# Performance work log

Hardware: AMD Instinct MI355X
Metric: run time of the kernel (lower is better)

The kernel has to match this reference:

```python
import jax, jax.numpy as jnp
import numpy as np

LAM = 0.5   # dec_init_lambda
NEG = -1e8  # attention mask fill


def gru_cell(x, h, W_ih, W_hh, b_ih, b_hh):
    # torch.nn.GRUCell math
    gi = x @ W_ih.T + b_ih
    gh = h @ W_hh.T + b_hh
    ir, iz, inn = jnp.split(gi, 3, axis=-1)
    hr, hz, hn = jnp.split(gh, 3, axis=-1)
    r = jax.nn.sigmoid(ir + hr)
    z = jax.nn.sigmoid(iz + hz)
    n = jnp.tanh(inn + r * hn)
    return (1.0 - z) * n + z * h


def setup_inputs() -> dict:
    key = jax.random.key(0)
    S, B, C, H, E, V, TY = 64, 64, 512, 512, 512, 32000, 49
    ks = jax.random.split(key, 16)
    sc = lambda d: 1.0 / float(np.sqrt(d))
    inp = {}
    inp['ctx'] = jax.random.normal(ks[0], (S, B, C), jnp.float32)
    inp['ctx_mask'] = jnp.ones((S, B), jnp.float32)
    inp['txt_ctx'] = jax.random.normal(ks[1], (B, C), jnp.float32)
    inp['y'] = jax.random.randint(ks[2], (TY, B), 0, V)
    emb = jax.random.normal(ks[3], (V, E), jnp.float32) * 0.01
    inp['emb_table'] = emb.at[0].set(0.0)  # padding_idx=0
    inp['W_ctx2ctx'] = jax.random.normal(ks[4], (C, C), jnp.float32) * sc(C)
    inp['W_hid2ctx'] = jax.random.normal(ks[5], (C, H), jnp.float32) * sc(H)
    inp['w_mlp'] = jax.random.normal(ks[6], (C,), jnp.float32) * sc(C)
    inp['W_ctx2hid'] = jax.random.normal(ks[7], (H, C), jnp.float32) * sc(C)
    inp['W_dec_init'] = jax.random.normal(ks[8], (H, C), jnp.float32) * sc(C)
    inp['W_ih0'] = jax.random.normal(ks[9], (3 * H, E), jnp.float32) * sc(E)
    inp['W_hh0'] = jax.random.normal(ks[10], (3 * H, H), jnp.float32) * sc(H)
    inp['b_ih0'] = jnp.zeros((3 * H,), jnp.float32)
    inp['b_hh0'] = jnp.zeros((3 * H,), jnp.float32)
    inp['W_ih1'] = jax.random.normal(ks[11], (3 * H, H), jnp.float32) * sc(H)
    inp['W_hh1'] = jax.random.normal(ks[12], (3 * H, H), jnp.float32) * sc(H)
    inp['b_ih1'] = jnp.zeros((3 * H,), jnp.float32)
    inp['b_hh1'] = jnp.zeros((3 * H,), jnp.float32)
    inp['W_hid2out'] = jax.random.normal(ks[13], (E, H), jnp.float32) * sc(H)
    inp['b_hid2out'] = jnp.zeros((E,), jnp.float32)  # bias_zero=True
    inp['W_out2prob'] = jax.random.normal(ks[14], (V, E), jnp.float32) * sc(E)
    inp['b_out2prob'] = jnp.zeros((V,), jnp.float32)
    return inp


def reference(ctx, ctx_mask, txt_ctx, y, emb_table,
              W_ctx2ctx, W_hid2ctx, w_mlp, W_ctx2hid, W_dec_init,
              W_ih0, W_hh0, b_ih0, b_hh0,
              W_ih1, W_hh1, b_ih1, b_hh1,
              W_hid2out, b_hid2out, W_out2prob, b_out2prob):
    # f_init: mix mean visual ctx with sentence ctx, project to h0
    mean_ctx = ctx.sum(0) / ctx_mask.sum(0)[:, None]          # (B, C)
    mixed = LAM * mean_ctx + (1.0 - LAM) * txt_ctx            # (B, C)
    h0 = jnp.tanh(mixed @ W_dec_init.T)                       # (B, H)

    # precompute ctx projection of MLP attention (ctx2ctx), shared across steps
    ctx_proj = jnp.einsum('sbc,mc->sbm', ctx, W_ctx2ctx)      # (S, B, C)

    x_seq = emb_table[y[:-1]]                                 # (T, B, E) teacher-forced inputs
    tgt = y[1:]                                               # (T, B) targets

    def step(h, xs):
        x, t = xs
        h1 = gru_cell(x, h, W_ih0, W_hh0, b_ih0, b_hh0)       # (B, H)
        q = h1 @ W_hid2ctx.T                                  # (B, C)
        scores = jnp.einsum('sbm,m->sb', jnp.tanh(ctx_proj + q[None]), w_mlp)
        scores = jnp.where(ctx_mask > 0, scores, NEG)
        alpha = jax.nn.softmax(scores, axis=0)                # (S, B) over source
        z_t = jnp.einsum('sb,sbc->bc', alpha, ctx) @ W_ctx2hid.T  # (B, H)
        h2 = gru_cell(z_t, h1, W_ih1, W_hh1, b_ih1, b_hh1)    # (B, H)
        logit = jnp.tanh(h2 @ W_hid2out.T + b_hid2out)        # (B, E)
        log_p = jax.nn.log_softmax(logit @ W_out2prob.T + b_out2prob, axis=-1)
        lp = jnp.take_along_axis(log_p, t[:, None], axis=1)[:, 0]
        loss_t = -jnp.where(t != 0, lp, 0.0).sum()            # NLLLoss(sum, ignore_index=0)
        return h2, loss_t

    _, losses = jax.lax.scan(step, h0, (x_seq, tgt))
    return losses.sum()
```

## Files before the change

### kernel.cpp

```cpp
#include <hip/hip_runtime.h>
#include <stdint.h>


using bf16x8 = __attribute__((ext_vector_type(8))) short;
using f32x4  = __attribute__((ext_vector_type(4))) float;
using s16x4  = __attribute__((ext_vector_type(4))) short;
typedef unsigned long long u64;
typedef unsigned int u32;

#define DI __device__ __forceinline__

DI short f2bf(float x){
  union { float f; uint32_t u; } v; v.f = x;
  uint32_t r = (v.u + 0x7FFFu + ((v.u >> 16) & 1u)) >> 16;
  return (short)r;
}
DI float bf2f(short s){
  union { uint32_t u; float f; } v; v.u = ((uint32_t)(unsigned short)s) << 16; return v.f;
}
DI float sigm(float x){ return __fdividef(1.f, 1.f + __expf(-x)); }
DI float ftanh(float x){ return 1.f - __fdividef(2.f, __expf(2.f*x) + 1.f); }
DI float wsum(float v){
  #pragma unroll
  for (int m = 32; m > 0; m >>= 1) v += __shfl_xor(v, m, 64);
  return v;
}
DI f32x4 mfma16(bf16x8 a, bf16x8 b, f32x4 c){
  return __builtin_amdgcn_mfma_f32_16x16x32_bf16(a, b, c, 0, 0, 0);
}

DI u32  ald32(const u32* p){ return __hip_atomic_load(p, __ATOMIC_RELAXED, __HIP_MEMORY_SCOPE_AGENT); }
DI void ast32(u32* p, u32 v){ __hip_atomic_store(p, v, __ATOMIC_RELAXED, __HIP_MEMORY_SCOPE_AGENT); }
DI u64  ald64(const u64* p){ return __hip_atomic_load(p, __ATOMIC_RELAXED, __HIP_MEMORY_SCOPE_AGENT); }
DI void ast64(u64* p, u64 v){ __hip_atomic_store(p, v, __ATOMIC_RELAXED, __HIP_MEMORY_SCOPE_AGENT); }
DI float aldf(const float* p){ return __hip_atomic_load(p, __ATOMIC_RELAXED, __HIP_MEMORY_SCOPE_AGENT); }
DI void astf(float* p, float v){ __hip_atomic_store(p, v, __ATOMIC_RELAXED, __HIP_MEMORY_SCOPE_AGENT); }

DI bf16x8 ldb(const short* __restrict__ W, int n0, int k0, int lane){
  return *(const bf16x8*)(W + (size_t)(n0 + (lane & 15)) * 512 + k0 + ((lane >> 4) << 3));
}

#define SLOT 64

DI void sig(u32* arr, int slot, u32 tok){
  if (threadIdx.x == 0){
    __builtin_amdgcn_s_waitcnt(0);
    ast32(arr + slot * SLOT, tok);
  }
}
DI void waitslots(const u32* arr, int base, int cnt, u32 tok){
  if (threadIdx.x < 64){
    for (;;){
      u32 v = (threadIdx.x < cnt) ? ald32(arr + (base + threadIdx.x) * SLOT) : tok;
      if (__all((int)(v - tok) >= 0)) break;
      __builtin_amdgcn_s_sleep(2);
    }
  }
  __syncthreads();
}


struct CvtJobs { const float* src[8]; short* dst[8]; int cum4[9]; };

__global__ __launch_bounds__(256) void k_cvt_multi(CvtJobs jb, int total4){
  int i = blockIdx.x * 256 + threadIdx.x;
  if (i >= total4) return;
  int j = 0;
  #pragma unroll
  for (int k = 0; k < 8; ++k) if (i >= jb.cum4[k + 1]) j = k + 1;
  int off = i - jb.cum4[j];
  float4 v = ((const float4*)jb.src[j])[off];
  s16x4 o; o[0] = f2bf(v.x); o[1] = f2bf(v.y); o[2] = f2bf(v.z); o[3] = f2bf(v.w);
  ((s16x4*)jb.dst[j])[off] = o;
}

__global__ __launch_bounds__(256) void k_tc(const float* __restrict__ W, short* __restrict__ WT){
  int i = blockIdx.x * 256 + threadIdx.x;
  int c = i >> 9, h = i & 511;
  WT[i] = f2bf(W[h * 512 + c]);
}

__global__ __launch_bounds__(256) void k_zero(float* __restrict__ p, int n){
  int i = blockIdx.x * 256 + threadIdx.x;
  if (i < n) p[i] = 0.f;
}

__global__ __launch_bounds__(256) void k_meanmix(const float* __restrict__ ctx, const float* __restrict__ mask,
                                                 const float* __restrict__ txt, float* __restrict__ mixed){
  int i = blockIdx.x * 256 + threadIdx.x;
  int b = i >> 9, c = i & 511;
  float s = 0.f;
  for (int t = 0; t < 64; ++t) s += ctx[(size_t)(t * 64 + b) * 512 + c];
  float dn = 0.f;
  for (int t = 0; t < 64; ++t) dn += mask[t * 64 + b];
  mixed[i] = 0.5f * (s / dn) + 0.5f * txt[i];
}

__global__ __launch_bounds__(256) void k_pack_h0(const float* __restrict__ h0, u32* __restrict__ hbf){
  int i = blockIdx.x * 256 + threadIdx.x;
  u32 lo = (u32)(unsigned short)f2bf(h0[2 * i]);
  u32 hi = (u32)(unsigned short)f2bf(h0[2 * i + 1]);
  hbf[i] = lo | (hi << 16);
}


DI bf16x8 load_a32(const float* __restrict__ A, int ld, int m0, int k0, int lane){
  const float* p = A + (size_t)(m0 + (lane & 15)) * ld + k0 + ((lane >> 4) << 3);
  bf16x8 f;
  #pragma unroll
  for (int j = 0; j < 8; ++j) f[j] = f2bf(p[j]);
  return f;
}

__global__ __launch_bounds__(256) void k_gemm_bt(const float* __restrict__ A, const short* __restrict__ W,
                                                 float* __restrict__ C, int N, int act){
  int wg = blockIdx.x * 4 + (threadIdx.x >> 6);
  int lane = threadIdx.x & 63;
  int ntiles = N >> 4;
  int mt = wg / ntiles, nt = wg - mt * ntiles;
  int m0 = mt << 4, n0 = nt << 4;
  f32x4 acc = {0.f, 0.f, 0.f, 0.f};
  for (int k = 0; k < 512; k += 32)
    acc = mfma16(load_a32(A, 512, m0, k, lane), ldb(W, n0, k, lane), acc);
  int col = n0 + (lane & 15);
  int r0 = m0 + ((lane >> 4) << 2);
  #pragma unroll
  for (int r = 0; r < 4; ++r){
    float v = acc[r];
    if (act) v = ftanh(v);
    C[(size_t)(r0 + r) * N + col] = v;
  }
}

__global__ __launch_bounds__(256) void k_gemm_bt_obf(const float* __restrict__ A, const short* __restrict__ W,
                                                     short* __restrict__ C, int N){
  int wg = blockIdx.x * 4 + (threadIdx.x >> 6);
  int lane = threadIdx.x & 63;
  int ntiles = N >> 4;
  int mt = wg / ntiles, nt = wg - mt * ntiles;
  int m0 = mt << 4, n0 = nt << 4;
  f32x4 acc = {0.f, 0.f, 0.f, 0.f};
  for (int k = 0; k < 512; k += 32)
    acc = mfma16(load_a32(A, 512, m0, k, lane), ldb(W, n0, k, lane), acc);
  int col = n0 + (lane & 15);
  int r0 = m0 + ((lane >> 4) << 2);
  #pragma unroll
  for (int r = 0; r < 4; ++r)
    C[(size_t)(r0 + r) * N + col] = f2bf(acc[r]);
}

__global__ __launch_bounds__(256) void k_gi0(const int* __restrict__ y, const float* __restrict__ emb,
                                             const short* __restrict__ W, const float* __restrict__ bias,
                                             float* __restrict__ C){
  int wg = blockIdx.x * 4 + (threadIdx.x >> 6);
  int lane = threadIdx.x & 63;
  int mt = wg / 96, nt = wg - mt * 96;
  int m0 = mt << 4, n0 = nt << 4;
  int yr = y[m0 + (lane & 15)];
  const float* arow = emb + (size_t)yr * 512;
  f32x4 acc = {0.f, 0.f, 0.f, 0.f};
  for (int k = 0; k < 512; k += 32){
    const float* p = arow + k + ((lane >> 4) << 3);
    bf16x8 a;
    #pragma unroll
    for (int j = 0; j < 8; ++j) a[j] = f2bf(p[j]);
    acc = mfma16(a, ldb(W, n0, k, lane), acc);
  }
  int col = n0 + (lane & 15);
  int r0 = m0 + ((lane >> 4) << 2);
  #pragma unroll
  for (int r = 0; r < 4; ++r)
    C[(size_t)(r0 + r) * 1536 + col] = acc[r] + bias[col];
}


struct RB {
  const float* gi0;
  const short* Whh0; const float* bhh0;
  const short* Whid2ctx;
  const short* Whh1; const float* bhh1;
  const short* Wcomb; const float* bih1;
  const short* ctx_proj;
  const float* ctx;
  const float* mask;
  const float* wmlp;
  unsigned short* h_bf;
  unsigned short* h1_bf;
  unsigned short* catt_bf;
  float* qpart;
  float* h2;
  u32* barA; u32* barC; u32* barD;
};

__global__ __launch_bounds__(256, 1) void k_recur(RB a){
  __shared__ unsigned short sH[16 * 520];
  __shared__ float sOut[16 * 64];
  __shared__ float qs[512];
  __shared__ float wm[512];
  __shared__ float sc[64], al[64];
  const int wg = blockIdx.x, tid = threadIdx.x;
  const int wv = tid >> 6, lane = tid & 63;

  wm[tid] = a.wmlp[tid]; wm[tid + 256] = a.wmlp[tid + 256];
  __syncthreads();

  auto burst16 = [&](const unsigned short* src, int row0){
    #pragma unroll
    for (int i = 0; i < 8; ++i){
      int idx = tid + i * 256;
      int r = idx >> 7, c4 = idx & 127;
      u64 v = ald64((const u64*)(src + (size_t)(row0 + r) * 512) + c4);
      *(u64*)(sH + r * 520 + c4 * 4) = v;
    }
    __syncthreads();
  };
  auto afrag = [&](int k0) -> bf16x8 {
    return *(const bf16x8*)(sH + (lane & 15) * 520 + k0 + ((lane >> 4) << 3));
  };
  auto packstore = [&](unsigned short* dst, int mrow0, int jbase){
    int r = tid >> 4, ch = tid & 15;
    float4 v = *(const float4*)&sOut[r * 64 + ch * 4];
    u64 pk = (u64)(unsigned short)f2bf(v.x)
           | ((u64)(unsigned short)f2bf(v.y) << 16)
           | ((u64)(unsigned short)f2bf(v.z) << 32)
           | ((u64)(unsigned short)f2bf(v.w) << 48);
    ast64((u64*)(dst + (size_t)(mrow0 + r) * 512 + jbase + ch * 4), pk);
  };
  auto attention = [&](int b){
    float q0 = 0.f, q1 = 0.f;
    #pragma unroll
    for (int cgi = 0; cgi < 8; ++cgi){
      u64 v = ald64((const u64*)(a.qpart + (size_t)(cgi * 64 + b) * 512) + tid);
      union { u64 u; float f[2]; } cv; cv.u = v;
      q0 += cv.f[0]; q1 += cv.f[1];
    }
    qs[2 * tid] = q0; qs[2 * tid + 1] = q1;
    __syncthreads();
    for (int i = 0; i < 16; ++i){
      int s = (wv << 4) + i;
      const short* cp = a.ctx_proj + (size_t)((s << 6) + b) * 512 + lane * 8;
      bf16x8 c8 = *(const bf16x8*)cp;
      float p = 0.f;
      #pragma unroll
      for (int j = 0; j < 8; ++j){
        int m = lane * 8 + j;
        p += ftanh(bf2f(c8[j]) + qs[m]) * wm[m];
      }
      p = wsum(p);
      if (lane == 0) sc[s] = p;
    }
    __syncthreads();
    if (tid < 64){
      float mk = a.mask[(tid << 6) + b];
      float v = (mk > 0.f) ? sc[tid] : -100000000.0f;
      float mx = v;
      #pragma unroll
      for (int m = 32; m > 0; m >>= 1) mx = fmaxf(mx, __shfl_xor(mx, m, 64));
      float e = __expf(v - mx);
      float se = e;
      #pragma unroll
      for (int m = 32; m > 0; m >>= 1) se += __shfl_xor(se, m, 64);
      al[tid] = e / se;
    }
    __syncthreads();
    float s0 = 0.f, s1 = 0.f;
    int c0 = tid * 2;
    for (int s = 0; s < 64; ++s){
      float2 cv = *(const float2*)(a.ctx + (size_t)((s << 6) + b) * 512 + c0);
      s0 += al[s] * cv.x; s1 += al[s] * cv.y;
    }
    u32 pk = (u32)(unsigned short)f2bf(s0) | ((u32)(unsigned short)f2bf(s1) << 16);
    ast32((u32*)a.catt_bf + (size_t)b * 256 + tid, pk);
  };

  if (wg < 32){
    const int rg = wg >> 3, cg = wg & 7;
    const int mrow0 = rg << 4, jbase = cg << 6;
    const int j0 = jbase + (wv << 4);
    const int col = j0 + (lane & 15), lcol = col - jbase;
    const int lr0 = (lane >> 4) << 2;
    const int batt = wg;
    const int abase = (batt >> 4) << 3;
    #pragma unroll 1
    for (int t = 0; t < 48; ++t){
      const u32 tok = t + 1;
      waitslots(a.barD, rg << 3, 8, (u32)t);
      burst16(a.h_bf, mrow0);
      const float* gi = a.gi0 + (size_t)t * 98304;
      float giv0[4], giv1[4], giv2[4];
      #pragma unroll
      for (int r = 0; r < 4; ++r){
        const float* gib = gi + (size_t)(mrow0 + lr0 + r) * 1536;
        giv0[r] = gib[col]; giv1[r] = gib[512 + col]; giv2[r] = gib[1024 + col];
      }
      f32x4 aR = {0,0,0,0}, aZ = {0,0,0,0}, aN = {0,0,0,0};
      for (int k0 = 0; k0 < 512; k0 += 32){
        bf16x8 af = afrag(k0);
        aR = mfma16(af, ldb(a.Whh0, j0,        k0, lane), aR);
        aZ = mfma16(af, ldb(a.Whh0, 512 + j0,  k0, lane), aZ);
        aN = mfma16(af, ldb(a.Whh0, 1024 + j0, k0, lane), aN);
      }
      #pragma unroll
      for (int r = 0; r < 4; ++r){
        int lr = lr0 + r;
        float rr = sigm(giv0[r] + aR[r] + a.bhh0[col]);
        float zz = sigm(giv1[r] + aZ[r] + a.bhh0[512 + col]);
        float nn = ftanh(giv2[r] + rr * (aN[r] + a.bhh0[1024 + col]));
        float hp = bf2f((short)sH[lr * 520 + col]);
        sOut[lr * 64 + lcol] = (1.f - zz) * nn + zz * hp;
      }
      __syncthreads();
      packstore(a.h1_bf, mrow0, jbase);
      bf16x8 qa0, qa1;
      #pragma unroll
      for (int j = 0; j < 8; ++j){
        qa0[j] = f2bf(sOut[(lane & 15) * 64 +      ((lane >> 4) << 3) + j]);
        qa1[j] = f2bf(sOut[(lane & 15) * 64 + 32 + ((lane >> 4) << 3) + j]);
      }
      #pragma unroll
      for (int nt = 0; nt < 8; ++nt){
        int n0 = (wv << 7) + (nt << 4);
        f32x4 qacc = {0,0,0,0};
        qacc = mfma16(qa0, ldb(a.Whid2ctx, n0, jbase,      lane), qacc);
        qacc = mfma16(qa1, ldb(a.Whid2ctx, n0, jbase + 32, lane), qacc);
        int qcol = n0 + (lane & 15);
        #pragma unroll
        for (int r = 0; r < 4; ++r)
          astf(a.qpart + (size_t)(cg * 64 + mrow0 + lr0 + r) * 512 + qcol, qacc[r]);
      }
      __syncthreads();
      sig(a.barA, wg, tok);
      waitslots(a.barA, abase, 8, tok);
      attention(batt);
      __syncthreads();
      sig(a.barC, batt, tok);
    }
  } else if (wg < 64){
    const int g = wg - 32;
    const int rg = g >> 3, cg = g & 7;
    const int mrow0 = rg << 4, jbase = cg << 6;
    const int j0 = jbase + (wv << 4);
    const int col = j0 + (lane & 15), lcol = col - jbase;
    const int lr0 = (lane >> 4) << 2;
    #pragma unroll 1
    for (int t = 0; t < 48; ++t){
      const u32 tok = t + 1;
      waitslots(a.barA, rg << 3, 8, tok);
      burst16(a.h1_bf, mrow0);
      f32x4 hR = {0,0,0,0}, hZ = {0,0,0,0}, hN = {0,0,0,0};
      for (int k0 = 0; k0 < 512; k0 += 32){
        bf16x8 af = afrag(k0);
        hR = mfma16(af, ldb(a.Whh1, j0,        k0, lane), hR);
        hZ = mfma16(af, ldb(a.Whh1, 512 + j0,  k0, lane), hZ);
        hN = mfma16(af, ldb(a.Whh1, 1024 + j0, k0, lane), hN);
      }
      float hp4[4];
      #pragma unroll
      for (int r = 0; r < 4; ++r) hp4[r] = bf2f((short)sH[(lr0 + r) * 520 + col]);
      waitslots(a.barC, mrow0, 16, tok);
      burst16(a.catt_bf, mrow0);
      f32x4 iR = {0,0,0,0}, iZ = {0,0,0,0}, iN = {0,0,0,0};
      for (int k0 = 0; k0 < 512; k0 += 32){
        bf16x8 af = afrag(k0);
        iR = mfma16(af, ldb(a.Wcomb, j0,        k0, lane), iR);
        iZ = mfma16(af, ldb(a.Wcomb, 512 + j0,  k0, lane), iZ);
        iN = mfma16(af, ldb(a.Wcomb, 1024 + j0, k0, lane), iN);
      }
      float* h2t = a.h2 + (size_t)t * 32768;
      #pragma unroll
      for (int r = 0; r < 4; ++r){
        int lr = lr0 + r, b = mrow0 + lr;
        float rr = sigm(iR[r] + a.bih1[col]        + hR[r] + a.bhh1[col]);
        float zz = sigm(iZ[r] + a.bih1[512 + col]  + hZ[r] + a.bhh1[512 + col]);
        float nn = ftanh(iN[r] + a.bih1[1024 + col] + rr * (hN[r] + a.bhh1[1024 + col]));
        float hv = (1.f - zz) * nn + zz * hp4[r];
        h2t[(size_t)b * 512 + col] = hv;
        sOut[lr * 64 + lcol] = hv;
      }
      __syncthreads();
      packstore(a.h_bf, mrow0, jbase);
      __syncthreads();
      sig(a.barD, g, tok);
    }
  } else {
    const int b = wg - 32;
    const int abase = (b >> 4) << 3;
    #pragma unroll 1
    for (int t = 0; t < 48; ++t){
      const u32 tok = t + 1;
      waitslots(a.barA, abase, 8, tok);
      attention(b);
      __syncthreads();
      sig(a.barC, b, tok);
    }
  }
}


__global__ __launch_bounds__(256) void k_logit(const float* __restrict__ A, const short* __restrict__ W,
                                               const float* __restrict__ bias, short* __restrict__ tlb,
                                               float* __restrict__ tlf){
  int wg = blockIdx.x * 4 + (threadIdx.x >> 6);
  int lane = threadIdx.x & 63;
  int mt = wg >> 5, nt = wg & 31;
  int m0 = mt << 4, n0 = nt << 4;
  f32x4 acc = {0.f, 0.f, 0.f, 0.f};
  for (int k = 0; k < 512; k += 32)
    acc = mfma16(load_a32(A, 512, m0, k, lane), ldb(W, n0, k, lane), acc);
  int col = n0 + (lane & 15);
  int r0 = m0 + ((lane >> 4) << 2);
  #pragma unroll
  for (int r = 0; r < 4; ++r){
    float v = ftanh(acc[r] + bias[col]);
    size_t o = (size_t)(r0 + r) * 512 + col;
    tlf[o] = v; tlb[o] = f2bf(v);
  }
}

__global__ __launch_bounds__(256) void k_sumexp(const short* __restrict__ A, const short* __restrict__ B,
                                                const float* __restrict__ bias, float* __restrict__ sumexp){
  __shared__ short lA[128 * 40];
  __shared__ short lB[128 * 40];
  int bm = blockIdx.x % 24, bn = blockIdx.x / 24;
  int m0 = bm * 128, n0 = bn * 128;
  int tid = threadIdx.x, w = tid >> 6, lane = tid & 63;
  int mq = (w >> 1) * 64, nq = (w & 1) * 64;
  f32x4 acc[4][4];
  #pragma unroll
  for (int i = 0; i < 4; ++i)
    #pragma unroll
    for (int j = 0; j < 4; ++j) acc[i][j] = (f32x4){0.f, 0.f, 0.f, 0.f};

  for (int k0 = 0; k0 < 512; k0 += 32){
    __syncthreads();
    #pragma unroll
    for (int i = 0; i < 2; ++i){
      int idx = tid * 8 + i * 2048;
      int row = idx >> 5, colh = idx & 31;
      *(bf16x8*)&lA[row * 40 + colh] = *(const bf16x8*)(A + (size_t)(m0 + row) * 512 + k0 + colh);
      *(bf16x8*)&lB[row * 40 + colh] = *(const bf16x8*)(B + (size_t)(n0 + row) * 512 + k0 + colh);
    }
    __syncthreads();
    bf16x8 af[4], bfr[4];
    #pragma unroll
    for (int x = 0; x < 4; ++x){
      af[x]  = *(const bf16x8*)&lA[(mq + x * 16 + (lane & 15)) * 40 + ((lane >> 4) << 3)];
      bfr[x] = *(const bf16x8*)&lB[(nq + x * 16 + (lane & 15)) * 40 + ((lane >> 4) << 3)];
    }
    #pragma unroll
    for (int mi = 0; mi < 4; ++mi)
      #pragma unroll
      for (int ni = 0; ni < 4; ++ni)
        acc[mi][ni] = mfma16(af[mi], bfr[ni], acc[mi][ni]);
  }

  #pragma unroll
  for (int mi = 0; mi < 4; ++mi){
    #pragma unroll
    for (int r = 0; r < 4; ++r){
      float e = 0.f;
      #pragma unroll
      for (int ni = 0; ni < 4; ++ni){
        int col = n0 + nq + ni * 16 + (lane & 15);
        e += __expf(acc[mi][ni][r] + bias[col]);
      }
      e += __shfl_xor(e, 1, 64); e += __shfl_xor(e, 2, 64);
      e += __shfl_xor(e, 4, 64); e += __shfl_xor(e, 8, 64);
      if ((lane & 15) == 0){
        int row = m0 + mq + mi * 16 + ((lane >> 4) << 2) + r;
        atomicAdd(&sumexp[row], e);
      }
    }
  }
}

__global__ __launch_bounds__(256) void k_loss(const float* __restrict__ tlf, const float* __restrict__ Wop,
                                              const float* __restrict__ bop, const int* __restrict__ y,
                                              const float* __restrict__ sumexp, float* __restrict__ loss){
  int step = blockIdx.x;
  int w = threadIdx.x >> 6, lane = threadIdx.x & 63;
  __shared__ float accw[4];
  float part = 0.f;
  for (int b = w; b < 64; b += 4){
    int row = step * 64 + b;
    int t = y[(step + 1) * 64 + b];
    if (t != 0){
      const float* a = tlf + (size_t)row * 512 + lane * 8;
      const float* wr = Wop + (size_t)t * 512 + lane * 8;
      float d = 0.f;
      #pragma unroll
      for (int j = 0; j < 8; ++j) d += a[j] * wr[j];
      d = wsum(d);
      if (lane == 0) part += d + bop[t] - __logf(sumexp[row]);
    }
  }
  if (lane == 0) accw[w] = part;
  __syncthreads();
  if (threadIdx.x == 0) atomicAdd(loss, -(accw[0] + accw[1] + accw[2] + accw[3]));
}

__global__ void k_final(const float* __restrict__ loss, float* __restrict__ out){
  if (threadIdx.x == 0 && blockIdx.x == 0) out[0] = loss[0];
}


extern "C" void kernel_launch(void* const* d_in, const int* in_sizes, int n_in,
                              void* d_out, int out_size, void* d_ws, size_t ws_size,
                              hipStream_t stream) {
  const float* ctx       = (const float*)d_in[0];
  const float* ctx_mask  = (const float*)d_in[1];
  const float* txt_ctx   = (const float*)d_in[2];
  const int*   y         = (const int*)d_in[3];
  const float* emb       = (const float*)d_in[4];
  const float* W_ctx2ctx = (const float*)d_in[5];
  const float* W_hid2ctx = (const float*)d_in[6];
  const float* w_mlp     = (const float*)d_in[7];
  const float* W_ctx2hid = (const float*)d_in[8];
  const float* W_dec_init= (const float*)d_in[9];
  const float* W_ih0     = (const float*)d_in[10];
  const float* W_hh0     = (const float*)d_in[11];
  const float* b_ih0     = (const float*)d_in[12];
  const float* b_hh0     = (const float*)d_in[13];
  const float* W_ih1     = (const float*)d_in[14];
  const float* W_hh1     = (const float*)d_in[15];
  const float* b_ih1     = (const float*)d_in[16];
  const float* b_hh1     = (const float*)d_in[17];
  const float* W_hid2out = (const float*)d_in[18];
  const float* b_hid2out = (const float*)d_in[19];
  const float* W_out2prob= (const float*)d_in[20];
  const float* b_out2prob= (const float*)d_in[21];
  float* out = (float*)d_out;

  char* p = (char*)d_ws;
  auto alloc = [&](size_t n){ char* r = p; p += (n + 255) & ~(size_t)255; return r; };
  short* Wb_hh0     = (short*)alloc((size_t)1536 * 512 * 2);
  short* Wb_hid2ctx = (short*)alloc((size_t)512 * 512 * 2);
  short* Wb_hh1     = (short*)alloc((size_t)1536 * 512 * 2);
  short* Wb_hid2out = (short*)alloc((size_t)512 * 512 * 2);
  short* Wb_dec     = (short*)alloc((size_t)512 * 512 * 2);
  short* Wb_c2c     = (short*)alloc((size_t)512 * 512 * 2);
  short* Wb_ih0     = (short*)alloc((size_t)1536 * 512 * 2);
  short* Wb_o2p     = (short*)alloc((size_t)32000 * 512 * 2);
  short* WctT       = (short*)alloc((size_t)512 * 512 * 2);
  short* Wb_comb    = (short*)alloc((size_t)1536 * 512 * 2);
  short* ctx_projbf = (short*)alloc((size_t)4096 * 512 * 2);
  float* gi0_all    = (float*)alloc((size_t)3072 * 1536 * 4);
  float* mixed      = (float*)alloc((size_t)64 * 512 * 4);
  float* h0buf      = (float*)alloc((size_t)64 * 512 * 4);
  unsigned short* h_bf    = (unsigned short*)alloc((size_t)64 * 512 * 2);
  unsigned short* h1_bf   = (unsigned short*)alloc((size_t)64 * 512 * 2);
  unsigned short* catt_bf = (unsigned short*)alloc((size_t)64 * 512 * 2);
  float* qpart      = (float*)alloc((size_t)8 * 64 * 512 * 4);
  float* h2_all     = (float*)alloc((size_t)3072 * 512 * 4);
  short* tl_bf      = (short*)alloc((size_t)3072 * 512 * 2);
  float* tl_f       = (float*)alloc((size_t)3072 * 512 * 4);
  int nbar = 3 * 64 * SLOT;
  float* zreg       = (float*)alloc((size_t)(3073 + nbar) * 4);
  float* sumexp     = zreg;
  float* lossbuf    = zreg + 3072;
  u32* barA         = (u32*)(zreg + 3073);
  u32* barC         = barA + 64 * SLOT;
  u32* barD         = barC + 64 * SLOT;

  dim3 blk(256);
  CvtJobs jb;
  const float* srcs[8] = {W_hh0, W_hid2ctx, W_hh1, W_hid2out, W_dec_init, W_ctx2ctx, W_ih0, W_out2prob};
  short* dsts[8] = {Wb_hh0, Wb_hid2ctx, Wb_hh1, Wb_hid2out, Wb_dec, Wb_c2c, Wb_ih0, Wb_o2p};
  int sizes4[8] = {1536*512/4, 512*512/4, 1536*512/4, 512*512/4, 512*512/4, 512*512/4, 1536*512/4, 32000*512/4};
  int cum = 0;
  for (int i = 0; i < 8; ++i){ jb.src[i] = srcs[i]; jb.dst[i] = dsts[i]; jb.cum4[i] = cum; cum += sizes4[i]; }
  jb.cum4[8] = cum;
  k_cvt_multi<<<dim3((cum + 255) / 256), blk, 0, stream>>>(jb, cum);
  k_tc<<<dim3(1024), blk, 0, stream>>>(W_ctx2hid, WctT);
  k_gemm_bt_obf<<<dim3(768), blk, 0, stream>>>(W_ih1, WctT, Wb_comb, 512);
  k_meanmix<<<dim3(128), blk, 0, stream>>>(ctx, ctx_mask, txt_ctx, mixed);
  k_gemm_bt<<<dim3(32), blk, 0, stream>>>(mixed, Wb_dec, h0buf, 512, 1);
  k_pack_h0<<<dim3(64), blk, 0, stream>>>(h0buf, (u32*)h_bf);
  k_gemm_bt_obf<<<dim3(2048), blk, 0, stream>>>(ctx, Wb_c2c, ctx_projbf, 512);
  k_gi0<<<dim3(4608), blk, 0, stream>>>(y, emb, Wb_ih0, b_ih0, gi0_all);
  k_zero<<<dim3((3073 + nbar + 255) / 256), blk, 0, stream>>>(zreg, 3073 + nbar);

  RB rb;
  rb.gi0 = gi0_all;
  rb.Whh0 = Wb_hh0; rb.bhh0 = b_hh0;
  rb.Whid2ctx = Wb_hid2ctx;
  rb.Whh1 = Wb_hh1; rb.bhh1 = b_hh1;
  rb.Wcomb = Wb_comb; rb.bih1 = b_ih1;
  rb.ctx_proj = ctx_projbf; rb.ctx = ctx; rb.mask = ctx_mask; rb.wmlp = w_mlp;
  rb.h_bf = h_bf; rb.h1_bf = h1_bf; rb.catt_bf = catt_bf;
  rb.qpart = qpart; rb.h2 = h2_all;
  rb.barA = barA; rb.barC = barC; rb.barD = barD;
  void* kargs[] = { &rb };
  hipLaunchCooperativeKernel((const void*)k_recur, dim3(96), blk, kargs, 0, stream);

  k_logit<<<dim3(1536), blk, 0, stream>>>(h2_all, Wb_hid2out, b_hid2out, tl_bf, tl_f);
  k_sumexp<<<dim3(6000), blk, 0, stream>>>(tl_bf, Wb_o2p, b_out2prob, sumexp);
  k_loss<<<dim3(48), blk, 0, stream>>>(tl_f, W_out2prob, b_out2prob, y, sumexp, lossbuf);
  k_final<<<dim3(1), blk, 0, stream>>>(lossbuf, out);
}
```

Measured before the change: 2.761 ms.

## Tune recurrent kernel: register-cached params, gi prefetch, LDS attention reduce, block swizzle

Several independent tweaks to the persistent recurrent kernel. Bias, w_mlp and mask values are loaded once into registers, and the next step's input-gate values are prefetched after the attention signal so the load is off the critical path. The per-source wave reductions are replaced by writing partial dot products to reused shared memory and summing rows per thread, and the spin-wait sleep is shortened. The sum-exp GEMM also gets a block-index swizzle meant to improve cache locality.

Result: faster. 2.552 ms (-7.6%).

```diff
diff --git a/kernel.cpp b/kernel.cpp
--- a/kernel.cpp
+++ b/kernel.cpp
@@ -53,7 +53,7 @@
     for (;;){
       u32 v = (threadIdx.x < cnt) ? ald32(arr + (base + threadIdx.x) * SLOT) : tok;
       if (__all((int)(v - tok) >= 0)) break;
-      __builtin_amdgcn_s_sleep(2);
+      __builtin_amdgcn_s_sleep(1);
     }
   }
   __syncthreads();
@@ -193,16 +193,14 @@
 };
 
 __global__ __launch_bounds__(256, 1) void k_recur(RB a){
-  __shared__ unsigned short sH[16 * 520];
-  __shared__ float sOut[16 * 64];
+  __shared__ char smem[16 * 520 * 2 + 16 * 64 * 4];
+  unsigned short* sH = (unsigned short*)smem;
+  float* sOut = (float*)(smem + 16 * 520 * 2);
+  float* pl   = (float*)smem;
   __shared__ float qs[512];
-  __shared__ float wm[512];
-  __shared__ float sc[64], al[64];
+  __shared__ float al[64];
   const int wg = blockIdx.x, tid = threadIdx.x;
   const int wv = tid >> 6, lane = tid & 63;
-
-  wm[tid] = a.wmlp[tid]; wm[tid + 256] = a.wmlp[tid + 256];
-  __syncthreads();
 
   auto burst16 = [&](const unsigned short* src, int row0){
     #pragma unroll
@@ -226,7 +224,7 @@
            | ((u64)(unsigned short)f2bf(v.w) << 48);
     ast64((u64*)(dst + (size_t)(mrow0 + r) * 512 + jbase + ch * 4), pk);
   };
-  auto attention = [&](int b){
+  auto attention = [&](int b, float maskv, const float (&w8)[8]){
     float q0 = 0.f, q1 = 0.f;
     #pragma unroll
     for (int cgi = 0; cgi < 8; ++cgi){
@@ -236,23 +234,28 @@
     }
     qs[2 * tid] = q0; qs[2 * tid + 1] = q1;
     __syncthreads();
+    float q8[8];
+    #pragma unroll
+    for (int j = 0; j < 8; ++j) q8[j] = qs[lane * 8 + j];
     for (int i = 0; i < 16; ++i){
       int s = (wv << 4) + i;
-      const short* cp = a.ctx_proj + (size_t)((s << 6) + b) * 512 + lane * 8;
-      bf16x8 c8 = *(const bf16x8*)cp;
+      bf16x8 c8 = *(const bf16x8*)(a.ctx_proj + (size_t)((s << 6) + b) * 512 + lane * 8);
       float p = 0.f;
       #pragma unroll
-      for (int j = 0; j < 8; ++j){
-        int m = lane * 8 + j;
-        p += ftanh(bf2f(c8[j]) + qs[m]) * wm[m];
-      }
-      p = wsum(p);
-      if (lane == 0) sc[s] = p;
+      for (int j = 0; j < 8; ++j)
+        p += ftanh(bf2f(c8[j]) + q8[j]) * w8[j];
+      pl[s * 65 + lane] = p;
     }
     __syncthreads();
     if (tid < 64){
-      float mk = a.mask[(tid << 6) + b];
-      float v = (mk > 0.f) ? sc[tid] : -100000000.0f;
+      const float* row = pl + tid * 65;
+      float v0 = 0.f, v1 = 0.f, v2 = 0.f, v3 = 0.f;
+      #pragma unroll
+      for (int j = 0; j < 64; j += 4){
+        v0 += row[j]; v1 += row[j + 1]; v2 += row[j + 2]; v3 += row[j + 3];
+      }
+      float v = (v0 + v1) + (v2 + v3);
+      v = (maskv > 0.f) ? v : -100000000.0f;
       float mx = v;
       #pragma unroll
       for (int m = 32; m > 0; m >>= 1) mx = fmaxf(mx, __shfl_xor(mx, m, 64));
@@ -281,18 +284,25 @@
     const int lr0 = (lane >> 4) << 2;
     const int batt = wg;
     const int abase = (batt >> 4) << 3;
+    const float bh0r = a.bhh0[col], bh0z = a.bhh0[512 + col], bh0n = a.bhh0[1024 + col];
+    float w8[8];
+    #pragma unroll
+    for (int j = 0; j < 8; ++j) w8[j] = a.wmlp[lane * 8 + j];
+    const float maskv = (tid < 64) ? a.mask[(tid << 6) + batt] : 0.f;
+    float g0[4], g1[4], g2[4];
+    {
+      const float* gi = a.gi0;
+      #pragma unroll
+      for (int r = 0; r < 4; ++r){
+        const float* gib = gi + (size_t)(mrow0 + lr0 + r) * 1536;
+        g0[r] = gib[col]; g1[r] = gib[512 + col]; g2[r] = gib[1024 + col];
+      }
+    }
     #pragma unroll 1
     for (int t = 0; t < 48; ++t){
       const u32 tok = t + 1;
       waitslots(a.barD, rg << 3, 8, (u32)t);
       burst16(a.h_bf, mrow0);
-      const float* gi = a.gi0 + (size_t)t * 98304;
-      float giv0[4], giv1[4], giv2[4];
-      #pragma unroll
-      for (int r = 0; r < 4; ++r){
-        const float* gib = gi + (size_t)(mrow0 + lr0 + r) * 1536;
-        giv0[r] = gib[col]; giv1[r] = gib[512 + col]; giv2[r] = gib[1024 + col];
-      }
       f32x4 aR = {0,0,0,0}, aZ = {0,0,0,0}, aN = {0,0,0,0};
       for (int k0 = 0; k0 < 512; k0 += 32){
         bf16x8 af = afrag(k0);
@@ -303,9 +313,9 @@
       #pragma unroll
       for (int r = 0; r < 4; ++r){
         int lr = lr0 + r;
-        float rr = sigm(giv0[r] + aR[r] + a.bhh0[col]);
-        float zz = sigm(giv1[r] + aZ[r] + a.bhh0[512 + col]);
-        float nn = ftanh(giv2[r] + rr * (aN[r] + a.bhh0[1024 + col]));
+        float rr = sigm(g0[r] + aR[r] + bh0r);
+        float zz = sigm(g1[r] + aZ[r] + bh0z);
+        float nn = ftanh(g2[r] + rr * (aN[r] + bh0n));
         float hp = bf2f((short)sH[lr * 520 + col]);
         sOut[lr * 64 + lcol] = (1.f - zz) * nn + zz * hp;
       }
@@ -331,9 +341,17 @@
       __syncthreads();
       sig(a.barA, wg, tok);
       waitslots(a.barA, abase, 8, tok);
-      attention(batt);
+      attention(batt, maskv, w8);
       __syncthreads();
       sig(a.barC, batt, tok);
+      if (t < 47){
+        const float* gi = a.gi0 + (size_t)(t + 1) * 98304;
+        #pragma unroll
+        for (int r = 0; r < 4; ++r){
+          const float* gib = gi + (size_t)(mrow0 + lr0 + r) * 1536;
+          g0[r] = gib[col]; g1[r] = gib[512 + col]; g2[r] = gib[1024 + col];
+        }
+      }
     }
   } else if (wg < 64){
     const int g = wg - 32;
@@ -342,6 +360,10 @@
     const int j0 = jbase + (wv << 4);
     const int col = j0 + (lane & 15), lcol = col - jbase;
     const int lr0 = (lane >> 4) << 2;
+    const float bcR = a.bih1[col]        + a.bhh1[col];
+    const float bcZ = a.bih1[512 + col]  + a.bhh1[512 + col];
+    const float biN = a.bih1[1024 + col];
+    const float bhN = a.bhh1[1024 + col];
     #pragma unroll 1
     for (int t = 0; t < 48; ++t){
       const u32 tok = t + 1;
@@ -370,9 +392,9 @@
       #pragma unroll
       for (int r = 0; r < 4; ++r){
         int lr = lr0 + r, b = mrow0 + lr;
-        float rr = sigm(iR[r] + a.bih1[col]        + hR[r] + a.bhh1[col]);
-        float zz = sigm(iZ[r] + a.bih1[512 + col]  + hZ[r] + a.bhh1[512 + col]);
-        float nn = ftanh(iN[r] + a.bih1[1024 + col] + rr * (hN[r] + a.bhh1[1024 + col]));
+        float rr = sigm(iR[r] + hR[r] + bcR);
+        float zz = sigm(iZ[r] + hZ[r] + bcZ);
+        float nn = ftanh(iN[r] + biN + rr * (hN[r] + bhN));
         float hv = (1.f - zz) * nn + zz * hp4[r];
         h2t[(size_t)b * 512 + col] = hv;
         sOut[lr * 64 + lcol] = hv;
@@ -385,11 +407,15 @@
   } else {
     const int b = wg - 32;
     const int abase = (b >> 4) << 3;
+    float w8[8];
+    #pragma unroll
+    for (int j = 0; j < 8; ++j) w8[j] = a.wmlp[lane * 8 + j];
+    const float maskv = (tid < 64) ? a.mask[(tid << 6) + b] : 0.f;
     #pragma unroll 1
     for (int t = 0; t < 48; ++t){
       const u32 tok = t + 1;
       waitslots(a.barA, abase, 8, tok);
-      attention(b);
+      attention(b, maskv, w8);
       __syncthreads();
       sig(a.barC, b, tok);
     }
@@ -421,7 +447,9 @@
                                                 const float* __restrict__ bias, float* __restrict__ sumexp){
   __shared__ short lA[128 * 40];
   __shared__ short lB[128 * 40];
-  int bm = blockIdx.x % 24, bn = blockIdx.x / 24;
+  int bid = blockIdx.x;
+  int swz = (bid & 7) * 750 + (bid >> 3);
+  int bm = swz % 24, bn = swz / 24;
   int m0 = bm * 128, n0 = bn * 128;
   int tid = threadIdx.x, w = tid >> 6, lane = tid & 63;
   int mq = (w >> 1) * 64, nq = (w & 1) * 64;
```
